# Optimization experiments

Measured on AMD Instinct MI355X. Metric: run time of the kernel, lower is better.

## Reference

```python
import jax, jax.numpy as jnp
import numpy as np

NUM_SP = 1024  # superpixel labels in [0, 1024); torch uses max(sp)+1 which equals this w.h.p.

def setup_inputs() -> dict:
    key = jax.random.key(0)
    k1, k2, k3 = jax.random.split(key, 3)
    features = jax.random.normal(k1, (1, 512, 512, 256), dtype=jnp.float32)
    superpixel = jax.random.randint(k2, (512, 512), 0, NUM_SP, dtype=jnp.int64)
    w_node = jax.random.normal(k3, (21, 256), dtype=jnp.float32) * 0.05
    return {"features": features, "superpixel": superpixel, "w_node": w_node}

def reference(features, superpixel, w_node):
    # features: (1, H, W, F); superpixel: (H, W) int; w_node: (C, F)
    n_feat = features.shape[-1]
    feats_flat = features.reshape(-1, n_feat)          # (H*W, F)
    sp_flat = superpixel.reshape(-1)                   # (H*W,)
    # L1-row-normalized one-hot matmul == per-superpixel mean (segment mean)
    sums = jax.ops.segment_sum(feats_flat, sp_flat, num_segments=NUM_SP)   # (num_sp, F)
    counts = jax.ops.segment_sum(jnp.ones_like(sp_flat, dtype=feats_flat.dtype),
                                 sp_flat, num_segments=NUM_SP)             # (num_sp,)
    node_features = sums / jnp.clip(counts, 1.0)[:, None]                  # empty sp -> 0, matches F.normalize eps
    # nn.Linear(n_feat, n_classes, bias=False): x @ W^T
    node_potentials = node_features @ w_node.T                             # (num_sp, C)
    return node_potentials
```

## Files before the change

### kernel.cpp

```cpp
#include <hip/hip_runtime.h>


#define NSP 1024
#define FDIM 256
#define G 4
#define CAP 1024

__global__ __launch_bounds__(1024, 4) void fused_segmean_linear_kernel(
    const float* __restrict__ feats, const int* __restrict__ sp,
    const float* __restrict__ wn, float* __restrict__ out, int n, int C) {
    __shared__ int list[G * CAP];
    __shared__ int cnt[G];
    __shared__ float part[16 * FDIM];
    __shared__ float mean_s[G * FDIM];

    const int b = blockIdx.x;
    const int t = (int)threadIdx.x;
    const int lane = t & 63;
    const int wave = t >> 6;

    if (t < G) cnt[t] = 0;
    __syncthreads();

    const int4* sp4 = (const int4*)sp;
    const int n4 = n >> 2;
    #pragma unroll 4
    for (int i = t; i < n4; i += 1024) {
        const int4 v = sp4[i];
        const int base = i << 2;
        if ((v.x >> 2) == b) { int p = atomicAdd(&cnt[v.x & 3], 1); if (p < CAP) list[(v.x & 3) * CAP + p] = base + 0; }
        if ((v.y >> 2) == b) { int p = atomicAdd(&cnt[v.y & 3], 1); if (p < CAP) list[(v.y & 3) * CAP + p] = base + 1; }
        if ((v.z >> 2) == b) { int p = atomicAdd(&cnt[v.z & 3], 1); if (p < CAP) list[(v.z & 3) * CAP + p] = base + 2; }
        if ((v.w >> 2) == b) { int p = atomicAdd(&cnt[v.w & 3], 1); if (p < CAP) list[(v.w & 3) * CAP + p] = base + 3; }
    }
    __syncthreads();

    const int g = wave >> 2;
    const int sub = wave & 3;
    const int ng = min(cnt[g], CAP);
    const int* mylist = &list[g * CAP];

    float a0x = 0.f, a0y = 0.f, a0z = 0.f, a0w = 0.f;
    float a1x = 0.f, a1y = 0.f, a1z = 0.f, a1w = 0.f;

    int pos = sub * 4;
    for (; pos + 3 < ng; pos += 16) {
        const int i0 = mylist[pos + 0];
        const int i1 = mylist[pos + 1];
        const int i2 = mylist[pos + 2];
        const int i3 = mylist[pos + 3];
        float4 v0 = ((const float4*)(feats + (size_t)i0 * FDIM))[lane];
        float4 v1 = ((const float4*)(feats + (size_t)i1 * FDIM))[lane];
        float4 v2 = ((const float4*)(feats + (size_t)i2 * FDIM))[lane];
        float4 v3 = ((const float4*)(feats + (size_t)i3 * FDIM))[lane];
        a0x += v0.x; a0y += v0.y; a0z += v0.z; a0w += v0.w;
        a1x += v1.x; a1y += v1.y; a1z += v1.z; a1w += v1.w;
        a0x += v2.x; a0y += v2.y; a0z += v2.z; a0w += v2.w;
        a1x += v3.x; a1y += v3.y; a1z += v3.z; a1w += v3.w;
    }
    for (; pos < ng; ++pos) {
        const int idx = mylist[pos];
        float4 v = ((const float4*)(feats + (size_t)idx * FDIM))[lane];
        a0x += v.x; a0y += v.y; a0z += v.z; a0w += v.w;
    }
    a0x += a1x; a0y += a1y; a0z += a1z; a0w += a1w;

    float4 pv; pv.x = a0x; pv.y = a0y; pv.z = a0z; pv.w = a0w;
    ((float4*)&part[wave * FDIM])[lane] = pv;
    __syncthreads();

    {
        const int gg = t >> 8;
        const int col = t & 255;
        float s = part[(gg * 4 + 0) * FDIM + col] +
                  part[(gg * 4 + 1) * FDIM + col] +
                  part[(gg * 4 + 2) * FDIM + col] +
                  part[(gg * 4 + 3) * FDIM + col];
        const int cg = cnt[gg];
        mean_s[gg * FDIM + col] = (cg > 0) ? s / (float)cg : 0.f;
    }
    __syncthreads();

    const float4 m = ((const float4*)&mean_s[g * FDIM])[lane];
    for (int c = sub; c < C; c += 4) {
        const float4 w4 = ((const float4*)(wn + (size_t)c * FDIM))[lane];
        float p = m.x * w4.x + m.y * w4.y + m.z * w4.z + m.w * w4.w;
        #pragma unroll
        for (int off = 32; off > 0; off >>= 1) p += __shfl_down(p, off, 64);
        if (lane == 0) out[(b * G + g) * C + c] = p;
    }
}

extern "C" void kernel_launch(void* const* d_in, const int* in_sizes, int n_in,
                              void* d_out, int out_size, void* d_ws,
                              size_t ws_size, hipStream_t stream) {
    const float* feats = (const float*)d_in[0];
    const int* sp = (const int*)d_in[1];
    const float* wn = (const float*)d_in[2];
    float* out = (float*)d_out;

    const int n_pix = in_sizes[1];
    const int C = in_sizes[2] / FDIM;

    fused_segmean_linear_kernel<<<NSP / G, 1024, 0, stream>>>(feats, sp, wn,
                                                              out, n_pix, C);
}
```

Before: 391.0 us.

## Overlap superpixel label scan with feature gather via chunked wave specialization

Splits the per-block label scan into four chunks. After the first chunk is scanned by all threads, waves 0-3 scan each following chunk while waves 4-15 gather and accumulate the feature rows already found. Waves are remapped so the group index is `wave & 3`, and the partial-sum reduction indexing is updated to match. Feature loads also switch to nontemporal vector loads. The aim is to hide gather latency behind the scan, at the cost of scanning three quarters of the labels with only a quarter of the threads and adding extra block-wide barriers.

```diff
diff --git a/kernel.cpp b/kernel.cpp
--- a/kernel.cpp
+++ b/kernel.cpp
@@ -5,12 +5,54 @@
 #define FDIM 256
 #define G 4
 #define CAP 1024
+#define NCHUNK 4
+
+typedef float f32x4 __attribute__((ext_vector_type(4)));
+
+__device__ __forceinline__ void scan_range(const int4* __restrict__ sp4,
+    int lo4, int hi4, int tid, int tstep, int b,
+    int* __restrict__ list, int* __restrict__ cnt)
+{
+    #pragma unroll 4
+    for (int i = lo4 + tid; i < hi4; i += tstep) {
+        const int4 v = sp4[i];
+        const int base = i << 2;
+        if ((v.x >> 2) == b) { int p = atomicAdd(&cnt[v.x & 3], 1); if (p < CAP) list[(v.x & 3) * CAP + p] = base + 0; }
+        if ((v.y >> 2) == b) { int p = atomicAdd(&cnt[v.y & 3], 1); if (p < CAP) list[(v.y & 3) * CAP + p] = base + 1; }
+        if ((v.z >> 2) == b) { int p = atomicAdd(&cnt[v.z & 3], 1); if (p < CAP) list[(v.z & 3) * CAP + p] = base + 2; }
+        if ((v.w >> 2) == b) { int p = atomicAdd(&cnt[v.w & 3], 1); if (p < CAP) list[(v.w & 3) * CAP + p] = base + 3; }
+    }
+}
+
+__device__ __forceinline__ void gather_range(const float* __restrict__ feats,
+    const int* __restrict__ mylist, int lo, int hi, int sidx, int stride,
+    int lane, f32x4& A0, f32x4& A1)
+{
+    int pos = lo + sidx * 4;
+    for (; pos + 3 < hi; pos += stride) {
+        const int i0 = mylist[pos + 0];
+        const int i1 = mylist[pos + 1];
+        const int i2 = mylist[pos + 2];
+        const int i3 = mylist[pos + 3];
+        f32x4 v0 = __builtin_nontemporal_load((const f32x4*)(feats + (size_t)i0 * FDIM) + lane);
+        f32x4 v1 = __builtin_nontemporal_load((const f32x4*)(feats + (size_t)i1 * FDIM) + lane);
+        f32x4 v2 = __builtin_nontemporal_load((const f32x4*)(feats + (size_t)i2 * FDIM) + lane);
+        f32x4 v3 = __builtin_nontemporal_load((const f32x4*)(feats + (size_t)i3 * FDIM) + lane);
+        A0 += v0; A1 += v1; A0 += v2; A1 += v3;
+    }
+    for (; pos < hi; ++pos) {
+        const int idx = mylist[pos];
+        f32x4 v = __builtin_nontemporal_load((const f32x4*)(feats + (size_t)idx * FDIM) + lane);
+        A0 += v;
+    }
+}
 
 __global__ __launch_bounds__(1024, 4) void fused_segmean_linear_kernel(
     const float* __restrict__ feats, const int* __restrict__ sp,
     const float* __restrict__ wn, float* __restrict__ out, int n, int C) {
     __shared__ int list[G * CAP];
     __shared__ int cnt[G];
+    __shared__ int lo_s[G], hi_s[G];
     __shared__ float part[16 * FDIM];
     __shared__ float mean_s[G * FDIM];
 
@@ -18,72 +60,58 @@
     const int t = (int)threadIdx.x;
     const int lane = t & 63;
     const int wave = t >> 6;
+    const int g = wave & 3;
+    const int sub = wave >> 2;
 
     if (t < G) cnt[t] = 0;
     __syncthreads();
 
     const int4* sp4 = (const int4*)sp;
     const int n4 = n >> 2;
-    #pragma unroll 4
-    for (int i = t; i < n4; i += 1024) {
-        const int4 v = sp4[i];
-        const int base = i << 2;
-        if ((v.x >> 2) == b) { int p = atomicAdd(&cnt[v.x & 3], 1); if (p < CAP) list[(v.x & 3) * CAP + p] = base + 0; }
-        if ((v.y >> 2) == b) { int p = atomicAdd(&cnt[v.y & 3], 1); if (p < CAP) list[(v.y & 3) * CAP + p] = base + 1; }
-        if ((v.z >> 2) == b) { int p = atomicAdd(&cnt[v.z & 3], 1); if (p < CAP) list[(v.z & 3) * CAP + p] = base + 2; }
-        if ((v.w >> 2) == b) { int p = atomicAdd(&cnt[v.w & 3], 1); if (p < CAP) list[(v.w & 3) * CAP + p] = base + 3; }
-    }
+    const int chunk = n4 / NCHUNK;
+
+    scan_range(sp4, 0, chunk, t, 1024, b, list, cnt);
+    __syncthreads();
+    if (t < G) { lo_s[t] = 0; hi_s[t] = min(cnt[t], CAP); }
     __syncthreads();
 
-    const int g = wave >> 2;
-    const int sub = wave & 3;
-    const int ng = min(cnt[g], CAP);
+    f32x4 A0 = {0.f, 0.f, 0.f, 0.f};
+    f32x4 A1 = {0.f, 0.f, 0.f, 0.f};
     const int* mylist = &list[g * CAP];
 
-    float a0x = 0.f, a0y = 0.f, a0z = 0.f, a0w = 0.f;
-    float a1x = 0.f, a1y = 0.f, a1z = 0.f, a1w = 0.f;
+    for (int c = 1; c < NCHUNK; ++c) {
+        if (wave < 4) {
+            const int end = (c == NCHUNK - 1) ? n4 : (c + 1) * chunk;
+            scan_range(sp4, c * chunk, end, t, 256, b, list, cnt);
+        } else {
+            gather_range(feats, mylist, lo_s[g], hi_s[g], sub - 1, 12, lane, A0, A1);
+        }
+        __syncthreads();
+        if (t < G) { lo_s[t] = hi_s[t]; hi_s[t] = min(cnt[t], CAP); }
+        __syncthreads();
+    }
 
-    int pos = sub * 4;
-    for (; pos + 3 < ng; pos += 16) {
-        const int i0 = mylist[pos + 0];
-        const int i1 = mylist[pos + 1];
-        const int i2 = mylist[pos + 2];
-        const int i3 = mylist[pos + 3];
-        float4 v0 = ((const float4*)(feats + (size_t)i0 * FDIM))[lane];
-        float4 v1 = ((const float4*)(feats + (size_t)i1 * FDIM))[lane];
-        float4 v2 = ((const float4*)(feats + (size_t)i2 * FDIM))[lane];
-        float4 v3 = ((const float4*)(feats + (size_t)i3 * FDIM))[lane];
-        a0x += v0.x; a0y += v0.y; a0z += v0.z; a0w += v0.w;
-        a1x += v1.x; a1y += v1.y; a1z += v1.z; a1w += v1.w;
-        a0x += v2.x; a0y += v2.y; a0z += v2.z; a0w += v2.w;
-        a1x += v3.x; a1y += v3.y; a1z += v3.z; a1w += v3.w;
-    }
-    for (; pos < ng; ++pos) {
-        const int idx = mylist[pos];
-        float4 v = ((const float4*)(feats + (size_t)idx * FDIM))[lane];
-        a0x += v.x; a0y += v.y; a0z += v.z; a0w += v.w;
-    }
-    a0x += a1x; a0y += a1y; a0z += a1z; a0w += a1w;
+    gather_range(feats, mylist, lo_s[g], hi_s[g], sub, 16, lane, A0, A1);
 
-    float4 pv; pv.x = a0x; pv.y = a0y; pv.z = a0z; pv.w = a0w;
-    ((float4*)&part[wave * FDIM])[lane] = pv;
+    A0 += A1;
+    ((f32x4*)&part[wave * FDIM])[lane] = A0;
     __syncthreads();
 
     {
         const int gg = t >> 8;
         const int col = t & 255;
-        float s = part[(gg * 4 + 0) * FDIM + col] +
-                  part[(gg * 4 + 1) * FDIM + col] +
-                  part[(gg * 4 + 2) * FDIM + col] +
-                  part[(gg * 4 + 3) * FDIM + col];
+        float s = part[(gg + 0) * FDIM + col] +
+                  part[(gg + 4) * FDIM + col] +
+                  part[(gg + 8) * FDIM + col] +
+                  part[(gg + 12) * FDIM + col];
         const int cg = cnt[gg];
         mean_s[gg * FDIM + col] = (cg > 0) ? s / (float)cg : 0.f;
     }
     __syncthreads();
 
-    const float4 m = ((const float4*)&mean_s[g * FDIM])[lane];
+    const f32x4 m = ((const f32x4*)&mean_s[g * FDIM])[lane];
     for (int c = sub; c < C; c += 4) {
-        const float4 w4 = ((const float4*)(wn + (size_t)c * FDIM))[lane];
+        const f32x4 w4 = ((const f32x4*)(wn + (size_t)c * FDIM))[lane];
         float p = m.x * w4.x + m.y * w4.y + m.z * w4.z + m.w * w4.w;
         #pragma unroll
         for (int off = 32; off > 0; off >>= 1) p += __shfl_down(p, off, 64);
```

Result: slower. 496.0 us (+26.8%).
